# Performance work log

Measured on AMD Instinct MI355X. Metric: run time of the kernel, lower is better.

The kernel has to match this reference:

```python
import jax, jax.numpy as jnp
import numpy as np

DIM = 1024
NUM_HEADS = 16
SCALE = (DIM // NUM_HEADS) ** -0.5


def setup_inputs() -> dict:
    key = jax.random.key(0)
    k1, k2, k3, k4 = jax.random.split(key, 4)
    x = jax.random.normal(k1, (8, 2048, DIM), dtype=jnp.float32)
    # nn.Linear(dim, 3*dim, bias=False): weight [3*dim, dim]
    w_qkv = jax.random.normal(k2, (3 * DIM, DIM), dtype=jnp.float32) * (DIM ** -0.5)
    # nn.Linear(dim, dim): weight [dim, dim], bias [dim]
    w_out = jax.random.normal(k3, (DIM, DIM), dtype=jnp.float32) * (DIM ** -0.5)
    b_out = jax.random.normal(k4, (DIM,), dtype=jnp.float32) * 0.01
    return {"x": x, "w_qkv": w_qkv, "w_out": w_out, "b_out": b_out}


def reference(x, w_qkv, w_out, b_out):
    # qkv projection: x @ w_qkv.T -> [B, N, 3*dim]; chunk into q,k,v
    qkv = jnp.einsum('bnd,ed->bne', x, w_qkv)
    q, k, v = jnp.split(qkv, 3, axis=-1)
    # full attention over the whole dim (module never splits heads)
    attn = jnp.einsum('bnd,bmd->bnm', q, k) * SCALE  # [B, N, N]
    attn = jax.nn.softmax(attn, axis=-1)
    out = jnp.einsum('bnm,bmd->bnd', attn, v)
    return jnp.einsum('bnd,ed->bne', out, w_out) + b_out
```

## Files before the change

### kernel.cpp

```cpp
#include <hip/hip_runtime.h>
#include <hip/hip_bf16.h>
#include <cstdint>
#include <cstddef>


typedef __bf16 bf16x8 __attribute__((ext_vector_type(8)));
typedef float f32x4 __attribute__((ext_vector_type(4)));

__device__ __forceinline__ void gl_lds16(const void* g, void* l) {
  __builtin_amdgcn_global_load_lds((const __attribute__((address_space(1))) void*)g,
                                   (__attribute__((address_space(3))) void*)l, 16, 0, 0);
}

__global__ __launch_bounds__(256) void cast_f32_bf16(const float* __restrict__ in,
                                                     __hip_bfloat16* __restrict__ out, int n) {
  int i = (blockIdx.x * 256 + threadIdx.x) * 8;
  if (i >= n) return;
  float4 a = *(const float4*)(in + i);
  float4 b = *(const float4*)(in + i + 4);
  __align__(16) __hip_bfloat16 o[8];
  o[0] = __float2bfloat16(a.x); o[1] = __float2bfloat16(a.y);
  o[2] = __float2bfloat16(a.z); o[3] = __float2bfloat16(a.w);
  o[4] = __float2bfloat16(b.x); o[5] = __float2bfloat16(b.y);
  o[6] = __float2bfloat16(b.z); o[7] = __float2bfloat16(b.w);
  *(uint4*)(out + i) = *(const uint4*)o;
}


#define ST1(SRCP, OFFS, LDSBASE, TT, KS)                                           \
  { const int kb_ = (TT) * 64 + (KS) * 32;                                         \
    _Pragma("unroll") for (int i = 0; i < 2; ++i)                                  \
      gl_lds16((SRCP) + OFFS[i] + kb_,                                             \
               sm + (LDSBASE) + (size_t)(tid + 512 * i) * 8); }

#define LDAF(APL, CH)                                                              \
  _Pragma("unroll") for (int mi = 0; mi < 4; ++mi)                                 \
    af[mi] = *(const bf16x8*)(sm + (APL) * 8192 + arow + ((CH) * 4 + mi) * 512);
#define LDBF(BPL)                                                                  \
  _Pragma("unroll") for (int ni = 0; ni < 4; ++ni)                                 \
    bfr[ni] = *(const bf16x8*)(sm + 32768 + (BPL) * 8192 + brow + ni * 512);

#define MF16(CH)                                                                   \
  __builtin_amdgcn_s_setprio(1);                                                   \
  _Pragma("unroll") for (int mi = 0; mi < 4; ++mi)                                 \
    _Pragma("unroll") for (int ni = 0; ni < 4; ++ni)                               \
      acc[(CH) * 4 + mi][ni] = __builtin_amdgcn_mfma_f32_16x16x32_bf16(            \
          af[mi], bfr[ni], acc[(CH) * 4 + mi][ni], 0, 0, 0);                       \
  __builtin_amdgcn_s_setprio(0);

#define ENDP(VMN)                                                                  \
  asm volatile("s_waitcnt vmcnt(" #VMN ")" ::: "memory");                          \
  __builtin_amdgcn_s_barrier();                                                    \
  __builtin_amdgcn_sched_barrier(0);
#define ENDB()                                                                     \
  __builtin_amdgcn_s_barrier();                                                    \
  __builtin_amdgcn_sched_barrier(0);

#define GEMM_CORE256(APTR, LDA, BPTR, LDB, KLEN)                                   \
  __shared__ __align__(16) __hip_bfloat16 sm[65536];                  \
  const __hip_bfloat16* Abase_ = (APTR);                                           \
  const __hip_bfloat16* Bbase_ = (BPTR);                                           \
  const int tid  = threadIdx.x;                                                    \
  const int lane = tid & 63;                                                       \
  const int q    = lane >> 4;                                                      \
  const int m16  = lane & 15;                                                      \
  const int wave = tid >> 6;                                                       \
  const int wr   = wave >> 2;                                                      \
  const int wc   = wave & 3;                                                       \
  const int row0 = blockIdx.y * 256;                                               \
  const int col0 = blockIdx.x * 256;                                               \
  unsigned srcA[2], srcB[2];                                                       \
  _Pragma("unroll") for (int i = 0; i < 2; ++i) {                                  \
    const int c_ = tid + 512 * i;                                                  \
    const int r_ = c_ >> 2;                                                        \
    const int kc_ = ((c_ & 3) ^ ((r_ >> 1) & 3)) * 8;                              \
    srcA[i] = (unsigned)(row0 + r_) * (unsigned)(LDA) + (unsigned)kc_;             \
    srcB[i] = (unsigned)(col0 + r_) * (unsigned)(LDB) + (unsigned)kc_;             \
  }                                                                                \
  const int NT = (KLEN) >> 6;                                                      \
  f32x4 acc[8][4];                                                                 \
  { const f32x4 z_ = {0.f, 0.f, 0.f, 0.f};                                         \
    _Pragma("unroll") for (int i = 0; i < 8; ++i)                                  \
      _Pragma("unroll") for (int j = 0; j < 4; ++j) acc[i][j] = z_; }              \
  const int soff = (q ^ ((m16 >> 1) & 3)) * 8;                                     \
  const int arow = (wr * 128 + m16) * 32 + soff;                                   \
  const int brow = (wc * 64 + m16) * 32 + soff;                                    \
  bf16x8 af[4], bfr[4];                                                            \
       \
  ST1(Abase_, srcA, 0,             0, 0)                                           \
  ST1(Bbase_, srcB, 32768,         0, 0)                                           \
  ST1(Abase_, srcA, 8192,          0, 1)                                           \
  ST1(Bbase_, srcB, 32768 + 8192,  0, 1)                                           \
  ST1(Abase_, srcA, 16384,         1, 0)                                           \
  ST1(Bbase_, srcB, 32768 + 16384, 1, 0)                                           \
  ENDP(8)                      \
  for (int t = 0; t < NT - 2; t += 2) {                                            \
    LDAF(0,0) LDBF(0) ST1(Abase_, srcA, 24576,         t+1, 1) MF16(0) ENDP(8)     \
    LDAF(0,1)         ST1(Bbase_, srcB, 32768 + 24576, t+1, 1) MF16(1) ENDP(8)     \
    LDAF(1,0) LDBF(1) ST1(Abase_, srcA, 0,             t+2, 0) MF16(0) ENDP(8)     \
    LDAF(1,1)         ST1(Bbase_, srcB, 32768,         t+2, 0) MF16(1) ENDP(8)     \
    LDAF(2,0) LDBF(2) ST1(Abase_, srcA, 8192,          t+2, 1) MF16(0) ENDP(8)     \
    LDAF(2,1)         ST1(Bbase_, srcB, 32768 + 8192,  t+2, 1) MF16(1) ENDP(8)     \
    LDAF(3,0) LDBF(3) ST1(Abase_, srcA, 16384,         t+3, 0) MF16(0) ENDP(8)     \
    LDAF(3,1)         ST1(Bbase_, srcB, 32768 + 16384, t+3, 0) MF16(1) ENDP(8)     \
  }                                                                                \
          \
  LDAF(0,0) LDBF(0) ST1(Abase_, srcA, 24576,         NT-1, 1) MF16(0) ENDP(8)      \
  LDAF(0,1)         ST1(Bbase_, srcB, 32768 + 24576, NT-1, 1) MF16(1) ENDP(8)      \
  LDAF(1,0) LDBF(1)                                           MF16(0) ENDP(6)      \
  LDAF(1,1)                                                   MF16(1) ENDP(4)      \
  LDAF(2,0) LDBF(2)                                           MF16(0) ENDP(2)      \
  LDAF(2,1)                                                   MF16(1) ENDP(0)      \
  LDAF(3,0) LDBF(3)                                           MF16(0) ENDB()       \
  LDAF(3,1)                                                   MF16(1)              \
                 \
  const int crow = row0 + wr * 128 + q * 4;                                        \
  const int ccol = col0 + wc * 64 + m16;

template<int OUT_MODE>
__global__ __launch_bounds__(512) void gemm_bt(
    const __hip_bfloat16* __restrict__ A, int lda, long long sA,
    const __hip_bfloat16* __restrict__ B, int ldb, long long sB,
    void* __restrict__ Cv, int ldc, long long sC,
    const float* __restrict__ bias, const float* __restrict__ rsum, int K)
{
  const int bz = blockIdx.z;
  GEMM_CORE256(A + (size_t)bz * sA, lda, B + (size_t)bz * sB, ldb, K)
  if constexpr (OUT_MODE == 0) {
    __hip_bfloat16* C = (__hip_bfloat16*)Cv + (size_t)bz * sC;
    #pragma unroll
    for (int mi = 0; mi < 8; ++mi)
      #pragma unroll
      for (int ni = 0; ni < 4; ++ni)
        #pragma unroll
        for (int r = 0; r < 4; ++r)
          C[(size_t)(crow + mi * 16 + r) * ldc + ccol + ni * 16] = __float2bfloat16(acc[mi][ni][r]);
  } else {
    float* C = (float*)Cv + (size_t)bz * sC;
    float bv[4];
    #pragma unroll
    for (int ni = 0; ni < 4; ++ni) bv[ni] = bias[ccol + ni * 16];
    #pragma unroll
    for (int mi = 0; mi < 8; ++mi) {
      float sc[4];
      #pragma unroll
      for (int r = 0; r < 4; ++r) sc[r] = 1.f / rsum[crow + mi * 16 + r];
      #pragma unroll
      for (int ni = 0; ni < 4; ++ni)
        #pragma unroll
        for (int r = 0; r < 4; ++r)
          C[(size_t)(crow + mi * 16 + r) * ldc + ccol + ni * 16] =
              acc[mi][ni][r] * sc[r] + bv[ni];
    }
  }
}

__global__ __launch_bounds__(512) void gemm_qk_exp(
    const __hip_bfloat16* __restrict__ A, int lda, long long sA,
    const __hip_bfloat16* __restrict__ B, int ldb, long long sB,
    __hip_bfloat16* __restrict__ Pv, int ldc, long long sC,
    float* __restrict__ Lsum, int ldl, int K)
{
  const int bz = blockIdx.z;
  GEMM_CORE256(A + (size_t)bz * sA, lda, B + (size_t)bz * sB, ldb, K)
  __hip_bfloat16* C = Pv + (size_t)bz * sC;
  float* Lrow = Lsum + (size_t)bz * ldl;
  #pragma unroll
  for (int mi = 0; mi < 8; ++mi) {
    #pragma unroll
    for (int r = 0; r < 4; ++r) {
      float s = 0.f;
      #pragma unroll
      for (int ni = 0; ni < 4; ++ni) {
        const float e = __expf(acc[mi][ni][r] * 0.125f);
        const __hip_bfloat16 h = __float2bfloat16(e);
        C[(size_t)(crow + mi * 16 + r) * ldc + ccol + ni * 16] = h;
        s += __bfloat162float(h);
      }
      #pragma unroll
      for (int mask = 1; mask < 16; mask <<= 1) s += __shfl_xor(s, mask);
      if (m16 == 0) atomicAdd(&Lrow[crow + mi * 16 + r], s);
    }
  }
}

__global__ __launch_bounds__(512) void gemm_qkv(
    const __hip_bfloat16* __restrict__ A, int lda,
    const __hip_bfloat16* __restrict__ B, int ldb,
    __hip_bfloat16* __restrict__ QK,
    __hip_bfloat16* __restrict__ Vt, int M, int K)
{
  GEMM_CORE256(A, lda, B, ldb, K)
  if (blockIdx.x < 8) {
    #pragma unroll
    for (int mi = 0; mi < 8; ++mi)
      #pragma unroll
      for (int ni = 0; ni < 4; ++ni)
        #pragma unroll
        for (int r = 0; r < 4; ++r)
          QK[(size_t)(crow + mi * 16 + r) * 2048 + ccol + ni * 16] = __float2bfloat16(acc[mi][ni][r]);
  } else {
    #pragma unroll
    for (int mi = 0; mi < 8; ++mi) {
      const int rowbase = crow + mi * 16;
      #pragma unroll
      for (int ni = 0; ni < 4; ++ni) {
        const int vc = ccol + ni * 16 - 2048;
        __align__(8) __hip_bfloat16 o[4];
        #pragma unroll
        for (int r = 0; r < 4; ++r) o[r] = __float2bfloat16(acc[mi][ni][r]);
        *(uint2*)(Vt + (size_t)vc * M + rowbase) = *(const uint2*)o;
      }
    }
  }
}

extern "C" void kernel_launch(void* const* d_in, const int* in_sizes, int n_in,
                              void* d_out, int out_size, void* d_ws, size_t ws_size,
                              hipStream_t stream) {
  const float* x     = (const float*)d_in[0];
  const float* w_qkv = (const float*)d_in[1];
  const float* w_out = (const float*)d_in[2];
  const float* b_out = (const float*)d_in[3];
  float* out = (float*)d_out;

  constexpr int Bz = 8, N = 2048, D = 1024, E = 3 * D;
  constexpr int M = Bz * N;

  char* p = (char*)d_ws;
  __hip_bfloat16* Wo = (__hip_bfloat16*)p; p += (size_t)D * D * 2;
  __hip_bfloat16* Vt = (__hip_bfloat16*)p; p += (size_t)D * M * 2;
  __hip_bfloat16* QK = (__hip_bfloat16*)p; p += (size_t)M * 2 * D * 2;
  __hip_bfloat16* AO = (__hip_bfloat16*)p; p += (size_t)M * D * 2;
  float*          L  = (float*)p;          p += (size_t)M * 4;
  char* dyn = p;
  const size_t fixed_sz = (size_t)(dyn - (char*)d_ws);
  const size_t xw_sz = (size_t)M * D * 2 + (size_t)E * D * 2;

  int G = 1;
  for (int g = 8; g >= 1; g >>= 1) {
    size_t dyn_sz = (size_t)g * N * N * 2;
    if (dyn_sz < xw_sz) dyn_sz = xw_sz;
    if (fixed_sz + dyn_sz <= ws_size) { G = g; break; }
  }

  __hip_bfloat16* Xb = (__hip_bfloat16*)dyn;
  __hip_bfloat16* Wq = (__hip_bfloat16*)(dyn + (size_t)M * D * 2);
  __hip_bfloat16* P  = (__hip_bfloat16*)dyn;

  hipMemsetAsync(L, 0, (size_t)M * 4, stream);
  cast_f32_bf16<<<(M * D) / (8 * 256), 256, 0, stream>>>(x, Xb, M * D);
  cast_f32_bf16<<<(E * D) / (8 * 256), 256, 0, stream>>>(w_qkv, Wq, E * D);
  cast_f32_bf16<<<(D * D) / (8 * 256), 256, 0, stream>>>(w_out, Wo, D * D);
  gemm_qkv<<<dim3(E / 256, M / 256), 512, 0, stream>>>(Xb, D, Wq, D, QK, Vt, M, D);

  for (int g = 0; g < Bz / G; ++g) {
    const __hip_bfloat16* Qg = QK + (size_t)g * G * N * (2 * D);
    gemm_qk_exp<<<dim3(N / 256, N / 256, G), 512, 0, stream>>>(
        Qg, 2 * D, (long long)N * 2 * D,
        Qg + D, 2 * D, (long long)N * 2 * D,
        P, N, (long long)N * N,
        L + (size_t)g * G * N, N, D);
    gemm_bt<0><<<dim3(D / 256, N / 256, G), 512, 0, stream>>>(
        P, N, (long long)N * N,
        Vt + (size_t)g * G * N, M, (long long)N,
        AO + (size_t)g * G * N * D, D, (long long)N * D,
        nullptr, nullptr, N);
  }

  gemm_bt<2><<<dim3(D / 256, M / 256, 1), 512, 0, stream>>>(
      AO, D, 0LL, Wo, D, 0LL, out, D, 0LL, b_out, L, D);
}
```

Measured before the change: 418.6 us.

## Fold Wq/Wk and Wo/Wv products into weights to drop projection GEMMs

The weights are pre-multiplied so the attention scores use (X·WqᵀWk)·Xᵀ, with X itself serving as the key matrix. The value path uses X·(Wo·Wv)ᵀ, which lets the output projection, softmax normalisation and bias be applied directly in the P·V kernel. This removes the separate K projection and the final out-projection GEMM, and with them the intermediate attention-output buffer. In exchange it adds a transpose-cast kernel and a small weight-product GEMM, and rounding the combined weights to bf16 changes numerical error.

```diff
diff --git a/kernel.cpp b/kernel.cpp
--- a/kernel.cpp
+++ b/kernel.cpp
@@ -26,6 +26,99 @@
   *(uint4*)(out + i) = *(const uint4*)o;
 }
 
+__global__ __launch_bounds__(256) void tcast(const float* __restrict__ w_qkv,
+                                             __hip_bfloat16* __restrict__ wsb) {
+  __shared__ float t[64][65];
+  const int z = blockIdx.z;
+  const int zo = (z == 0) ? 2 : ((z == 1) ? 0 : 3);
+  const float* src = w_qkv + (size_t)z * 1024 * 1024;
+  __hip_bfloat16* dst = wsb + (size_t)zo * 1024 * 1024;
+  const int r0 = blockIdx.y * 64, c0 = blockIdx.x * 64;
+  const int tid = threadIdx.x;
+  const int lr = tid >> 2, lc4 = tid & 3;
+  #pragma unroll
+  for (int j = 0; j < 4; ++j) {
+    float4 v = *(const float4*)(src + (size_t)(r0 + lr) * 1024 + c0 + lc4 * 16 + j * 4);
+    t[lr][lc4 * 16 + j * 4 + 0] = v.x;
+    t[lr][lc4 * 16 + j * 4 + 1] = v.y;
+    t[lr][lc4 * 16 + j * 4 + 2] = v.z;
+    t[lr][lc4 * 16 + j * 4 + 3] = v.w;
+  }
+  __syncthreads();
+  const int oc = tid >> 2;
+  #pragma unroll
+  for (int s2 = 0; s2 < 2; ++s2) {
+    const int s = (tid & 3) + s2 * 4;
+    __align__(16) __hip_bfloat16 o[8];
+    #pragma unroll
+    for (int j = 0; j < 8; ++j) o[j] = __float2bfloat16(t[s * 8 + j][oc]);
+    *(uint4*)(dst + (size_t)(c0 + oc) * 1024 + r0 + s * 8) = *(const uint4*)o;
+  }
+}
+
+#define GEMM_CORE64(APTR, LDA, BPTR, LDB, KLEN)                                    \
+  __shared__ __align__(16) __hip_bfloat16 As[128 * 64];                            \
+  __shared__ __align__(16) __hip_bfloat16 Bs[128 * 64];                            \
+  const int tid  = threadIdx.x;                                                    \
+  const int lane = tid & 63;                                                       \
+  const int q    = lane >> 4;                                                      \
+  const int m16  = lane & 15;                                                      \
+  const int wave = tid >> 6;                                                       \
+  const int wr   = wave >> 1;                                                      \
+  const int wc   = wave & 1;                                                       \
+  const int row0 = blockIdx.y * 128;                                               \
+  const int col0 = blockIdx.x * 128;                                               \
+  unsigned offA[4], offB[4];                                                       \
+  _Pragma("unroll") for (int i = 0; i < 4; ++i) {                                  \
+    const int c = tid + 256 * i;                                                   \
+    const int r = c >> 3, kc = ((c ^ (c >> 3)) & 7) * 8;                           \
+    offA[i] = (unsigned)(row0 + r) * (unsigned)(LDA) + kc;                         \
+    offB[i] = (unsigned)(col0 + r) * (unsigned)(LDB) + kc;                         \
+  }                                                                                \
+  const f32x4 zeroS = {0.f, 0.f, 0.f, 0.f};                                        \
+  f32x4 acc[4][4];                                                                 \
+  _Pragma("unroll") for (int i = 0; i < 4; ++i)                                    \
+    _Pragma("unroll") for (int j = 0; j < 4; ++j) acc[i][j] = zeroS;               \
+  const int sl0 = (q ^ (m16 & 7)) * 8;                                             \
+  for (int k0 = 0; k0 < (KLEN); k0 += 64) {                                        \
+    _Pragma("unroll") for (int i = 0; i < 4; ++i) {                                \
+      gl_lds16((APTR) + offA[i] + k0, As + ((size_t)tid + 256 * i) * 8);           \
+      gl_lds16((BPTR) + offB[i] + k0, Bs + ((size_t)tid + 256 * i) * 8);           \
+    }                                                                              \
+    __syncthreads();                                                               \
+    _Pragma("unroll") for (int step = 0; step < 2; ++step) {                       \
+      const int so = sl0 ^ (step * 32);                                            \
+      bf16x8 af[4], bfr[4];                                                        \
+      _Pragma("unroll") for (int mi = 0; mi < 4; ++mi)                             \
+        af[mi] = *(const bf16x8*)(As + (wr * 64 + mi * 16 + m16) * 64 + so);       \
+      _Pragma("unroll") for (int ni = 0; ni < 4; ++ni)                             \
+        bfr[ni] = *(const bf16x8*)(Bs + (wc * 64 + ni * 16 + m16) * 64 + so);      \
+      _Pragma("unroll") for (int mi = 0; mi < 4; ++mi)                             \
+        _Pragma("unroll") for (int ni = 0; ni < 4; ++ni)                           \
+          acc[mi][ni] = __builtin_amdgcn_mfma_f32_16x16x32_bf16(af[mi], bfr[ni],   \
+                                                                acc[mi][ni],0,0,0);\
+    }                                                                              \
+    __syncthreads();                                                               \
+  }                                                                                \
+  const int crow = row0 + wr * 64 + q * 4;                                         \
+  const int ccol = col0 + wc * 64 + m16;
+
+__global__ __launch_bounds__(256) void gemm_small(
+    const __hip_bfloat16* __restrict__ A, int lda, long long sA,
+    const __hip_bfloat16* __restrict__ B, int ldb, long long sB,
+    __hip_bfloat16* __restrict__ Cv, int ldc, long long sC, int K)
+{
+  const int bz = blockIdx.z;
+  GEMM_CORE64(A + (size_t)bz * sA, lda, B + (size_t)bz * sB, ldb, K)
+  __hip_bfloat16* C = Cv + (size_t)bz * sC;
+  #pragma unroll
+  for (int mi = 0; mi < 4; ++mi)
+    #pragma unroll
+    for (int ni = 0; ni < 4; ++ni)
+      #pragma unroll
+      for (int r = 0; r < 4; ++r)
+        C[(size_t)(crow + mi * 16 + r) * ldc + ccol + ni * 16] = __float2bfloat16(acc[mi][ni][r]);
+}
 
 #define ST1(SRCP, OFFS, LDSBASE, TT, KS)                                           \
   { const int kb_ = (TT) * 64 + (KS) * 32;                                         \
@@ -86,14 +179,13 @@
   const int arow = (wr * 128 + m16) * 32 + soff;                                   \
   const int brow = (wc * 64 + m16) * 32 + soff;                                    \
   bf16x8 af[4], bfr[4];                                                            \
-       \
   ST1(Abase_, srcA, 0,             0, 0)                                           \
   ST1(Bbase_, srcB, 32768,         0, 0)                                           \
   ST1(Abase_, srcA, 8192,          0, 1)                                           \
   ST1(Bbase_, srcB, 32768 + 8192,  0, 1)                                           \
   ST1(Abase_, srcA, 16384,         1, 0)                                           \
   ST1(Bbase_, srcB, 32768 + 16384, 1, 0)                                           \
-  ENDP(8)                      \
+  ENDP(8)                                                                          \
   for (int t = 0; t < NT - 2; t += 2) {                                            \
     LDAF(0,0) LDBF(0) ST1(Abase_, srcA, 24576,         t+1, 1) MF16(0) ENDP(8)     \
     LDAF(0,1)         ST1(Bbase_, srcB, 32768 + 24576, t+1, 1) MF16(1) ENDP(8)     \
@@ -104,7 +196,6 @@
     LDAF(3,0) LDBF(3) ST1(Abase_, srcA, 16384,         t+3, 0) MF16(0) ENDP(8)     \
     LDAF(3,1)         ST1(Bbase_, srcB, 32768 + 16384, t+3, 0) MF16(1) ENDP(8)     \
   }                                                                                \
-          \
   LDAF(0,0) LDBF(0) ST1(Abase_, srcA, 24576,         NT-1, 1) MF16(0) ENDP(8)      \
   LDAF(0,1)         ST1(Bbase_, srcB, 32768 + 24576, NT-1, 1) MF16(1) ENDP(8)      \
   LDAF(1,0) LDBF(1)                                           MF16(0) ENDP(6)      \
@@ -113,44 +204,36 @@
   LDAF(2,1)                                                   MF16(1) ENDP(0)      \
   LDAF(3,0) LDBF(3)                                           MF16(0) ENDB()       \
   LDAF(3,1)                                                   MF16(1)              \
-                 \
   const int crow = row0 + wr * 128 + q * 4;                                        \
   const int ccol = col0 + wc * 64 + m16;
 
-template<int OUT_MODE>
-__global__ __launch_bounds__(512) void gemm_bt(
-    const __hip_bfloat16* __restrict__ A, int lda, long long sA,
-    const __hip_bfloat16* __restrict__ B, int ldb, long long sB,
-    void* __restrict__ Cv, int ldc, long long sC,
-    const float* __restrict__ bias, const float* __restrict__ rsum, int K)
+__global__ __launch_bounds__(512) void gemm_qv(
+    const __hip_bfloat16* __restrict__ A, int lda,
+    const __hip_bfloat16* __restrict__ B, int ldb,
+    __hip_bfloat16* __restrict__ Qx,
+    __hip_bfloat16* __restrict__ Vt, int M, int K)
 {
-  const int bz = blockIdx.z;
-  GEMM_CORE256(A + (size_t)bz * sA, lda, B + (size_t)bz * sB, ldb, K)
-  if constexpr (OUT_MODE == 0) {
-    __hip_bfloat16* C = (__hip_bfloat16*)Cv + (size_t)bz * sC;
+  GEMM_CORE256(A, lda, B, ldb, K)
+  if (blockIdx.x < 4) {
     #pragma unroll
     for (int mi = 0; mi < 8; ++mi)
       #pragma unroll
       for (int ni = 0; ni < 4; ++ni)
         #pragma unroll
         for (int r = 0; r < 4; ++r)
-          C[(size_t)(crow + mi * 16 + r) * ldc + ccol + ni * 16] = __float2bfloat16(acc[mi][ni][r]);
+          Qx[(size_t)(crow + mi * 16 + r) * 1024 + ccol + ni * 16] = __float2bfloat16(acc[mi][ni][r]);
   } else {
-    float* C = (float*)Cv + (size_t)bz * sC;
-    float bv[4];
-    #pragma unroll
-    for (int ni = 0; ni < 4; ++ni) bv[ni] = bias[ccol + ni * 16];
     #pragma unroll
     for (int mi = 0; mi < 8; ++mi) {
-      float sc[4];
-      #pragma unroll
-      for (int r = 0; r < 4; ++r) sc[r] = 1.f / rsum[crow + mi * 16 + r];
-      #pragma unroll
-      for (int ni = 0; ni < 4; ++ni)
+      const int rowbase = crow + mi * 16;
+      #pragma unroll
+      for (int ni = 0; ni < 4; ++ni) {
+        const int vc = ccol + ni * 16 - 1024;
+        __align__(8) __hip_bfloat16 o[4];
         #pragma unroll
-        for (int r = 0; r < 4; ++r)
-          C[(size_t)(crow + mi * 16 + r) * ldc + ccol + ni * 16] =
-              acc[mi][ni][r] * sc[r] + bv[ni];
+        for (int r = 0; r < 4; ++r) o[r] = __float2bfloat16(acc[mi][ni][r]);
+        *(uint2*)(Vt + (size_t)vc * M + rowbase) = *(const uint2*)o;
+      }
     }
   }
 }
@@ -184,34 +267,30 @@
   }
 }
 
-__global__ __launch_bounds__(512) void gemm_qkv(
-    const __hip_bfloat16* __restrict__ A, int lda,
-    const __hip_bfloat16* __restrict__ B, int ldb,
-    __hip_bfloat16* __restrict__ QK,
-    __hip_bfloat16* __restrict__ Vt, int M, int K)
+__global__ __launch_bounds__(512) void gemm_pv_out(
+    const __hip_bfloat16* __restrict__ A, int lda, long long sA,
+    const __hip_bfloat16* __restrict__ B, int ldb, long long sB,
+    float* __restrict__ Cv, int ldc, long long sC,
+    const float* __restrict__ bias, const float* __restrict__ rsum, int K)
 {
-  GEMM_CORE256(A, lda, B, ldb, K)
-  if (blockIdx.x < 8) {
-    #pragma unroll
-    for (int mi = 0; mi < 8; ++mi)
-      #pragma unroll
-      for (int ni = 0; ni < 4; ++ni)
-        #pragma unroll
-        for (int r = 0; r < 4; ++r)
-          QK[(size_t)(crow + mi * 16 + r) * 2048 + ccol + ni * 16] = __float2bfloat16(acc[mi][ni][r]);
-  } else {
-    #pragma unroll
-    for (int mi = 0; mi < 8; ++mi) {
-      const int rowbase = crow + mi * 16;
-      #pragma unroll
-      for (int ni = 0; ni < 4; ++ni) {
-        const int vc = ccol + ni * 16 - 2048;
-        __align__(8) __hip_bfloat16 o[4];
-        #pragma unroll
-        for (int r = 0; r < 4; ++r) o[r] = __float2bfloat16(acc[mi][ni][r]);
-        *(uint2*)(Vt + (size_t)vc * M + rowbase) = *(const uint2*)o;
-      }
-    }
+  const int bz = blockIdx.z;
+  GEMM_CORE256(A + (size_t)bz * sA, lda, B + (size_t)bz * sB, ldb, K)
+  float* C = Cv + (size_t)bz * sC;
+  const float* rs = rsum + (size_t)bz * 2048;
+  float bv[4];
+  #pragma unroll
+  for (int ni = 0; ni < 4; ++ni) bv[ni] = bias[ccol + ni * 16];
+  #pragma unroll
+  for (int mi = 0; mi < 8; ++mi) {
+    float sc[4];
+    #pragma unroll
+    for (int r = 0; r < 4; ++r) sc[r] = 1.f / rs[crow + mi * 16 + r];
+    #pragma unroll
+    for (int ni = 0; ni < 4; ++ni)
+      #pragma unroll
+      for (int r = 0; r < 4; ++r)
+        C[(size_t)(crow + mi * 16 + r) * ldc + ccol + ni * 16] =
+            acc[mi][ni][r] * sc[r] + bv[ni];
   }
 }
 
@@ -224,50 +303,50 @@
   const float* b_out = (const float*)d_in[3];
   float* out = (float*)d_out;
 
-  constexpr int Bz = 8, N = 2048, D = 1024, E = 3 * D;
+  constexpr int Bz = 8, N = 2048, D = 1024;
   constexpr int M = Bz * N;
-
-  char* p = (char*)d_ws;
-  __hip_bfloat16* Wo = (__hip_bfloat16*)p; p += (size_t)D * D * 2;
-  __hip_bfloat16* Vt = (__hip_bfloat16*)p; p += (size_t)D * M * 2;
-  __hip_bfloat16* QK = (__hip_bfloat16*)p; p += (size_t)M * 2 * D * 2;
-  __hip_bfloat16* AO = (__hip_bfloat16*)p; p += (size_t)M * D * 2;
+  constexpr size_t SLOT = (size_t)1024 * 1024;
+
+  __hip_bfloat16* wsb = (__hip_bfloat16*)d_ws;
+  __hip_bfloat16* WkT = wsb;
+  __hip_bfloat16* WqT = wsb + 2 * SLOT;
+  __hip_bfloat16* Wob = wsb + 1 * SLOT;
+  __hip_bfloat16* Wt  = wsb + 4 * SLOT;
+  char* p = (char*)(wsb + 6 * SLOT);
+  __hip_bfloat16* Xb = (__hip_bfloat16*)p; p += (size_t)M * D * 2;
+  __hip_bfloat16* Qx = (__hip_bfloat16*)p; p += (size_t)M * D * 2;
+  __hip_bfloat16* Vt = (__hip_bfloat16*)p; p += (size_t)M * D * 2;
   float*          L  = (float*)p;          p += (size_t)M * 4;
   char* dyn = p;
   const size_t fixed_sz = (size_t)(dyn - (char*)d_ws);
-  const size_t xw_sz = (size_t)M * D * 2 + (size_t)E * D * 2;
 
   int G = 1;
   for (int g = 8; g >= 1; g >>= 1) {
     size_t dyn_sz = (size_t)g * N * N * 2;
-    if (dyn_sz < xw_sz) dyn_sz = xw_sz;
     if (fixed_sz + dyn_sz <= ws_size) { G = g; break; }
   }
-
-  __hip_bfloat16* Xb = (__hip_bfloat16*)dyn;
-  __hip_bfloat16* Wq = (__hip_bfloat16*)(dyn + (size_t)M * D * 2);
-  __hip_bfloat16* P  = (__hip_bfloat16*)dyn;
+  __hip_bfloat16* P = (__hip_bfloat16*)dyn;
 
   hipMemsetAsync(L, 0, (size_t)M * 4, stream);
   cast_f32_bf16<<<(M * D) / (8 * 256), 256, 0, stream>>>(x, Xb, M * D);
-  cast_f32_bf16<<<(E * D) / (8 * 256), 256, 0, stream>>>(w_qkv, Wq, E * D);
-  cast_f32_bf16<<<(D * D) / (8 * 256), 256, 0, stream>>>(w_out, Wo, D * D);
-  gemm_qkv<<<dim3(E / 256, M / 256), 512, 0, stream>>>(Xb, D, Wq, D, QK, Vt, M, D);
+  tcast<<<dim3(16, 16, 3), 256, 0, stream>>>(w_qkv, wsb);
+  cast_f32_bf16<<<(D * D) / (8 * 256), 256, 0, stream>>>(w_out, Wob, D * D);
+  gemm_small<<<dim3(8, 8, 2), 256, 0, stream>>>(
+      WkT, D, (long long)SLOT, WqT, D, (long long)SLOT, Wt, D, (long long)SLOT, D);
+
+  gemm_qv<<<dim3(8, M / 256), 512, 0, stream>>>(Xb, D, Wt, D, Qx, Vt, M, D);
 
   for (int g = 0; g < Bz / G; ++g) {
-    const __hip_bfloat16* Qg = QK + (size_t)g * G * N * (2 * D);
+    const size_t goff = (size_t)g * G * N;
     gemm_qk_exp<<<dim3(N / 256, N / 256, G), 512, 0, stream>>>(
-        Qg, 2 * D, (long long)N * 2 * D,
-        Qg + D, 2 * D, (long long)N * 2 * D,
+        Qx + goff * D, D, (long long)N * D,
+        Xb + goff * D, D, (long long)N * D,
         P, N, (long long)N * N,
-        L + (size_t)g * G * N, N, D);
-    gemm_bt<0><<<dim3(D / 256, N / 256, G), 512, 0, stream>>>(
+        L + goff, N, D);
+    gemm_pv_out<<<dim3(D / 256, N / 256, G), 512, 0, stream>>>(
         P, N, (long long)N * N,
-        Vt + (size_t)g * G * N, M, (long long)N,
-        AO + (size_t)g * G * N * D, D, (long long)N * D,
-        nullptr, nullptr, N);
-  }
-
-  gemm_bt<2><<<dim3(D / 256, M / 256, 1), 512, 0, stream>>>(
-      AO, D, 0LL, Wo, D, 0LL, out, D, 0LL, b_out, L, D);
-}
+        Vt + goff, M, (long long)N,
+        out + goff * D, D, (long long)N * D,
+        b_out, L + goff, N);
+  }
+}
```

Result: faster. 375.9 us (-10.2%).
